# Kernel optimization log

Hardware: AMD Instinct MI355X
Metric: run time of the kernel (lower is better)

Reference implementation:

```python
import jax, jax.numpy as jnp
import numpy as np

N = 100000
E = 1600000
NIN = 128
NOUT = 128


def setup_inputs() -> dict:
    key = jax.random.key(0)
    k1, k2, k3, k4 = jax.random.split(key, 4)
    x = jax.random.normal(k1, (N, NIN), dtype=jnp.float32)
    edge_index = jax.random.randint(k2, (2, E), 0, N, dtype=jnp.int64)
    edge_attr = jnp.ones((E,), dtype=jnp.float32)  # unused by GCNConv
    # PyG Linear weight is [out, in]; glorot-ish init
    W = jax.random.normal(k3, (NOUT, NIN), dtype=jnp.float32) / np.sqrt(NIN)
    b = jnp.zeros((NOUT,), dtype=jnp.float32)
    return {"x": x, "edge_index": edge_index, "edge_attr": edge_attr, "W": W, "b": b}


def reference(x, edge_index, edge_attr, W, b):
    # PyG GCNConv: add self-loops, symmetric degree normalization,
    # linear transform, scatter-add aggregation at destination, + bias.
    n = x.shape[0]
    loops = jnp.arange(n, dtype=edge_index.dtype)
    src = jnp.concatenate([edge_index[0], loops])  # [E+N]
    dst = jnp.concatenate([edge_index[1], loops])  # [E+N]
    # degree over destination (col) including self-loops, edge weight = 1
    deg = jax.ops.segment_sum(jnp.ones_like(dst, dtype=x.dtype), dst, num_segments=n)
    dinv = jnp.where(deg > 0, jax.lax.rsqrt(deg), 0.0)
    norm = dinv[src] * dinv[dst]  # [E+N]
    h = x @ W.T  # [N, NOUT]
    msg = h[src] * norm[:, None]  # [E+N, NOUT]
    out = jax.ops.segment_sum(msg, dst, num_segments=n)  # [N, NOUT]
    return out + b
```

## Files before the change

### kernel.cpp

```cpp
#include <hip/hip_runtime.h>

#define TPB 256
#define NSCAT 256
#define BSH 5
#define BCAP 1024
#define MAXBUK 3200

typedef __attribute__((ext_vector_type(4))) float f32x4;
typedef __attribute__((ext_vector_type(8))) short short8;

__device__ __forceinline__ unsigned short f2bf(float f) {
    unsigned u = __float_as_uint(f);
    u = (u + 0x7fffu + ((u >> 16) & 1u)) >> 16;
    return (unsigned short)u;
}
__device__ __forceinline__ float bflo(unsigned u) { return __uint_as_float(u << 16); }
__device__ __forceinline__ float bfhi(unsigned u) { return __uint_as_float(u & 0xffff0000u); }


__global__ __launch_bounds__(256) void k_scatgemm(
    const int* __restrict__ src, const int* __restrict__ dst,
    int* __restrict__ bcur, unsigned* __restrict__ packed,
    const float* __restrict__ x, const float* __restrict__ W,
    unsigned short* __restrict__ g, int N, int E, int NBUK)
{
    __shared__ __align__(16) char smem[34816];
    const int t = threadIdx.x;

    if (blockIdx.x < NSCAT) {
        int* cnt = (int*)smem;
        int* cur = cnt + MAXBUK;
        for (int i = t; i < NBUK; i += 256) cnt[i] = 0;
        __syncthreads();
        const int chunk = (E + NSCAT - 1) / NSCAT;
        const int lo = blockIdx.x * chunk;
        const int hi = min(E, lo + chunk);
        for (int e = lo + t; e < hi; e += 256)
            atomicAdd(&cnt[dst[e] >> BSH], 1);
        __syncthreads();
        for (int i = t; i < NBUK; i += 256) {
            int c = cnt[i];
            cur[i] = i * BCAP + (c ? atomicAdd(&bcur[i], c) : 0);
        }
        __syncthreads();
        for (int e = lo + t; e < hi; e += 256) {
            int d = dst[e];
            int bkt = d >> BSH;
            int pos = atomicAdd(&cur[bkt], 1);
            if (pos < bkt * BCAP + BCAP)
                packed[pos] = ((unsigned)src[e] << 8) | (unsigned)(d & 31);
        }
    } else {
        typedef unsigned short wb_t[136];
        wb_t* wb = (wb_t*)smem;

        for (int ch = t; ch < 2048; ch += 256) {
            int nrow = ch >> 4, k8 = (ch & 15) << 3;
            const float* wp = W + nrow * 128 + k8;
            float4 w0 = *(const float4*)wp;
            float4 w1 = *(const float4*)(wp + 4);
            union { unsigned short u[8]; uint4 q; } pk;
            pk.u[0] = f2bf(w0.x); pk.u[1] = f2bf(w0.y); pk.u[2] = f2bf(w0.z); pk.u[3] = f2bf(w0.w);
            pk.u[4] = f2bf(w1.x); pk.u[5] = f2bf(w1.y); pk.u[6] = f2bf(w1.z); pk.u[7] = f2bf(w1.w);
            *(uint4*)&wb[nrow][k8] = pk.q;
        }
        __syncthreads();

        const int lane = t & 63;
        const int wid  = t >> 6;
        const int l15  = lane & 15;
        const int quad = lane >> 4;
        const int row  = (blockIdx.x - NSCAT) * 64 + wid * 16 + l15;
        const int rowc = (row < N) ? row : (N - 1);

        f32x4 acc[8];
        #pragma unroll
        for (int u = 0; u < 8; ++u) acc[u] = (f32x4){0.f, 0.f, 0.f, 0.f};

        #pragma unroll
        for (int ks = 0; ks < 4; ++ks) {
            const int kb = ks * 32 + quad * 8;
            float4 a0 = *(const float4*)(x + (long)rowc * 128 + kb);
            float4 a1 = *(const float4*)(x + (long)rowc * 128 + kb + 4);
            union { unsigned short u[8]; short8 v; } af;
            af.u[0] = f2bf(a0.x); af.u[1] = f2bf(a0.y); af.u[2] = f2bf(a0.z); af.u[3] = f2bf(a0.w);
            af.u[4] = f2bf(a1.x); af.u[5] = f2bf(a1.y); af.u[6] = f2bf(a1.z); af.u[7] = f2bf(a1.w);
            #pragma unroll
            for (int u = 0; u < 8; ++u) {
                short8 bf = *(const short8*)&wb[u * 16 + l15][kb];
                acc[u] = __builtin_amdgcn_mfma_f32_16x16x32_bf16(bf, af.v, acc[u], 0, 0, 0);
            }
        }

        if (row < N) {
            unsigned short* gp = g + (long)row * 128 + quad * 4;
            #pragma unroll
            for (int u = 0; u < 8; ++u) {
                unsigned short u0 = f2bf(acc[u][0]);
                unsigned short u1 = f2bf(acc[u][1]);
                unsigned short u2 = f2bf(acc[u][2]);
                unsigned short u3 = f2bf(acc[u][3]);
                uint2 pk;
                pk.x = (unsigned)u0 | ((unsigned)u1 << 16);
                pk.y = (unsigned)u2 | ((unsigned)u3 << 16);
                *(uint2*)(gp + u * 16) = pk;
            }
        }
    }
}


__global__ __launch_bounds__(256) void k_dinv(const unsigned* __restrict__ packed,
                                              const int* __restrict__ bcur,
                                              float* __restrict__ dinv, int N) {
    __shared__ int hist[32];
    const int b = blockIdx.x;
    const int t = threadIdx.x;
    if (t < 32) hist[t] = 0;
    __syncthreads();
    const int cnt = min(bcur[b], BCAP);
    const int base = b * BCAP;
    for (int e = t; e < cnt; e += 256)
        atomicAdd(&hist[packed[base + e] & 31u], 1);
    __syncthreads();
    if (t < 32) {
        int d = (b << BSH) + t;
        if (d < N) dinv[d] = rsqrtf((float)hist[t] + 1.0f);
    }
}


__global__ __launch_bounds__(256) void k_aggsort(const unsigned* __restrict__ packed,
                                                 const int* __restrict__ bcur,
                                                 const float* __restrict__ dinv,
                                                 const unsigned short* __restrict__ g,
                                                 const float* __restrict__ b_,
                                                 float* __restrict__ out, int N) {
    __shared__ int hist[32], lbase[32], scur[32];
    __shared__ unsigned stage[BCAP];
    const int b = blockIdx.x;
    const int t = threadIdx.x;
    if (t < 32) hist[t] = 0;
    __syncthreads();
    const int cnt = min(bcur[b], BCAP);
    const int base = b * BCAP;
    for (int e = t; e < cnt; e += 256)
        atomicAdd(&hist[packed[base + e] & 31u], 1);
    __syncthreads();
    if (t < 32) {
        int v = hist[t];
        int incl = v;
        #pragma unroll
        for (int d = 1; d < 32; d <<= 1) {
            int o = __shfl_up(incl, d);
            if (t >= d) incl += o;
        }
        lbase[t] = incl - v;
        scur[t]  = incl - v;
    }
    __syncthreads();
    for (int e = t; e < cnt; e += 256) {
        unsigned pk = packed[base + e];
        int pos = atomicAdd(&scur[pk & 31u], 1);
        stage[pos] = pk & 0xffffff00u;
    }
    __syncthreads();

    const int c = (t & 31) << 2;
    const char* gb = (const char*)g + (c << 1);
    #pragma unroll 1
    for (int round = 0; round < 4; ++round) {
        const int dl = round * 8 + (t >> 5);
        const int d  = (b << BSH) + dl;
        if (d >= N) continue;

        float4 acc = make_float4(0.f, 0.f, 0.f, 0.f);
        auto addrow = [&](unsigned off) {
            float dv = dinv[off >> 8];
            uint2 p = *(const uint2*)(gb + off);
            acc.x = fmaf(bflo(p.x), dv, acc.x);
            acc.y = fmaf(bfhi(p.x), dv, acc.y);
            acc.z = fmaf(bflo(p.y), dv, acc.z);
            acc.w = fmaf(bfhi(p.y), dv, acc.w);
        };

        addrow((unsigned)d << 8);
        int e  = lbase[dl];
        int s1 = e + hist[dl];
        for (; e + 8 <= s1; e += 8) {
            unsigned a[8];
            #pragma unroll
            for (int j = 0; j < 8; ++j) a[j] = stage[e + j];
            #pragma unroll
            for (int j = 0; j < 8; ++j) addrow(a[j]);
        }
        for (; e + 4 <= s1; e += 4) {
            unsigned a[4];
            #pragma unroll
            for (int j = 0; j < 4; ++j) a[j] = stage[e + j];
            #pragma unroll
            for (int j = 0; j < 4; ++j) addrow(a[j]);
        }
        for (; e < s1; ++e) addrow(stage[e]);

        float s = rsqrtf((float)hist[dl] + 1.0f);
        float4 bb = *(const float4*)(b_ + c);
        float4 r = make_float4(acc.x * s + bb.x, acc.y * s + bb.y,
                               acc.z * s + bb.z, acc.w * s + bb.w);
        *(float4*)(out + (long)d * 128 + c) = r;
    }
}


extern "C" void kernel_launch(void* const* d_in, const int* in_sizes, int n_in,
                              void* d_out, int out_size, void* d_ws, size_t ws_size,
                              hipStream_t stream) {
    const float* x  = (const float*)d_in[0];
    const int*   ei = (const int*)d_in[1];
    const float* W  = (const float*)d_in[3];
    const float* b  = (const float*)d_in[4];
    float* out = (float*)d_out;

    const int N = in_sizes[0] / 128;
    const int E = in_sizes[1] / 2;
    const int* src = ei;
    const int* dst = ei + E;
    const int NBUK = (N + 31) >> BSH;

    char* p = (char*)d_ws;
    auto carve = [&](size_t bytes) { char* q = p; p += (bytes + 255) & ~(size_t)255; return q; };
    int*            bcur   = (int*)           carve((size_t)MAXBUK * 4);
    float*          dinv   = (float*)         carve((size_t)N * 4);
    unsigned*       packed = (unsigned*)      carve((size_t)MAXBUK * BCAP * 4);
    unsigned short* g      = (unsigned short*)carve((size_t)N * 128 * 2);

    const int gemmBlocks = (N + 63) / 64;

    hipMemsetAsync(bcur, 0, (size_t)NBUK * 4, stream);

    k_scatgemm<<<NSCAT + gemmBlocks, TPB, 0, stream>>>(src, dst, bcur, packed,
                                                       x, W, g, N, E, NBUK);
    k_dinv    <<<NBUK, TPB, 0, stream>>>(packed, bcur, dinv, N);
    k_aggsort <<<NBUK, TPB, 0, stream>>>(packed, bcur, dinv, g, b, out, N);
}
```

Baseline: 230.5 us.

## Halve shared memory by staging W in two halves and reusing scatter buffer

Cuts the kernel's static shared memory in half. The scatter path now keeps bucket counts and cursors in a single array, and the GEMM path converts and stages W into LDS one 64-row half at a time, with an extra pair of barriers per half. The x row fragments are loaded and converted once up front and held in registers. The aim is higher occupancy (more resident blocks per CU); the cost is extra synchronisation and more live registers.

```diff
diff --git a/kernel.cpp b/kernel.cpp
--- a/kernel.cpp
+++ b/kernel.cpp
@@ -24,47 +24,34 @@
     const float* __restrict__ x, const float* __restrict__ W,
     unsigned short* __restrict__ g, int N, int E, int NBUK)
 {
-    __shared__ __align__(16) char smem[34816];
+    __shared__ __align__(16) char smem[17408];
     const int t = threadIdx.x;
 
     if (blockIdx.x < NSCAT) {
-        int* cnt = (int*)smem;
-        int* cur = cnt + MAXBUK;
-        for (int i = t; i < NBUK; i += 256) cnt[i] = 0;
+        int* a = (int*)smem;
+        for (int i = t; i < NBUK; i += 256) a[i] = 0;
         __syncthreads();
         const int chunk = (E + NSCAT - 1) / NSCAT;
         const int lo = blockIdx.x * chunk;
         const int hi = min(E, lo + chunk);
         for (int e = lo + t; e < hi; e += 256)
-            atomicAdd(&cnt[dst[e] >> BSH], 1);
+            atomicAdd(&a[dst[e] >> BSH], 1);
         __syncthreads();
         for (int i = t; i < NBUK; i += 256) {
-            int c = cnt[i];
-            cur[i] = i * BCAP + (c ? atomicAdd(&bcur[i], c) : 0);
+            int c = a[i];
+            a[i] = i * BCAP + (c ? atomicAdd(&bcur[i], c) : 0);
         }
         __syncthreads();
         for (int e = lo + t; e < hi; e += 256) {
             int d = dst[e];
             int bkt = d >> BSH;
-            int pos = atomicAdd(&cur[bkt], 1);
+            int pos = atomicAdd(&a[bkt], 1);
             if (pos < bkt * BCAP + BCAP)
                 packed[pos] = ((unsigned)src[e] << 8) | (unsigned)(d & 31);
         }
     } else {
         typedef unsigned short wb_t[136];
         wb_t* wb = (wb_t*)smem;
-
-        for (int ch = t; ch < 2048; ch += 256) {
-            int nrow = ch >> 4, k8 = (ch & 15) << 3;
-            const float* wp = W + nrow * 128 + k8;
-            float4 w0 = *(const float4*)wp;
-            float4 w1 = *(const float4*)(wp + 4);
-            union { unsigned short u[8]; uint4 q; } pk;
-            pk.u[0] = f2bf(w0.x); pk.u[1] = f2bf(w0.y); pk.u[2] = f2bf(w0.z); pk.u[3] = f2bf(w0.w);
-            pk.u[4] = f2bf(w1.x); pk.u[5] = f2bf(w1.y); pk.u[6] = f2bf(w1.z); pk.u[7] = f2bf(w1.w);
-            *(uint4*)&wb[nrow][k8] = pk.q;
-        }
-        __syncthreads();
 
         const int lane = t & 63;
         const int wid  = t >> 6;
@@ -73,23 +60,46 @@
         const int row  = (blockIdx.x - NSCAT) * 64 + wid * 16 + l15;
         const int rowc = (row < N) ? row : (N - 1);
 
-        f32x4 acc[8];
-        #pragma unroll
-        for (int u = 0; u < 8; ++u) acc[u] = (f32x4){0.f, 0.f, 0.f, 0.f};
-
+        short8 af[4];
         #pragma unroll
         for (int ks = 0; ks < 4; ++ks) {
             const int kb = ks * 32 + quad * 8;
             float4 a0 = *(const float4*)(x + (long)rowc * 128 + kb);
             float4 a1 = *(const float4*)(x + (long)rowc * 128 + kb + 4);
-            union { unsigned short u[8]; short8 v; } af;
-            af.u[0] = f2bf(a0.x); af.u[1] = f2bf(a0.y); af.u[2] = f2bf(a0.z); af.u[3] = f2bf(a0.w);
-            af.u[4] = f2bf(a1.x); af.u[5] = f2bf(a1.y); af.u[6] = f2bf(a1.z); af.u[7] = f2bf(a1.w);
-            #pragma unroll
-            for (int u = 0; u < 8; ++u) {
-                short8 bf = *(const short8*)&wb[u * 16 + l15][kb];
-                acc[u] = __builtin_amdgcn_mfma_f32_16x16x32_bf16(bf, af.v, acc[u], 0, 0, 0);
+            union { unsigned short u[8]; short8 v; } cf;
+            cf.u[0] = f2bf(a0.x); cf.u[1] = f2bf(a0.y); cf.u[2] = f2bf(a0.z); cf.u[3] = f2bf(a0.w);
+            cf.u[4] = f2bf(a1.x); cf.u[5] = f2bf(a1.y); cf.u[6] = f2bf(a1.z); cf.u[7] = f2bf(a1.w);
+            af[ks] = cf.v;
+        }
+
+        f32x4 acc[8];
+        #pragma unroll
+        for (int u = 0; u < 8; ++u) acc[u] = (f32x4){0.f, 0.f, 0.f, 0.f};
+
+        #pragma unroll
+        for (int half = 0; half < 2; ++half) {
+            for (int ch = t; ch < 1024; ch += 256) {
+                int nrow = ch >> 4, k8 = (ch & 15) << 3;
+                const float* wp = W + (half * 64 + nrow) * 128 + k8;
+                float4 w0 = *(const float4*)wp;
+                float4 w1 = *(const float4*)(wp + 4);
+                union { unsigned short u[8]; uint4 q; } pk;
+                pk.u[0] = f2bf(w0.x); pk.u[1] = f2bf(w0.y); pk.u[2] = f2bf(w0.z); pk.u[3] = f2bf(w0.w);
+                pk.u[4] = f2bf(w1.x); pk.u[5] = f2bf(w1.y); pk.u[6] = f2bf(w1.z); pk.u[7] = f2bf(w1.w);
+                *(uint4*)&wb[nrow][k8] = pk.q;
             }
+            __syncthreads();
+            #pragma unroll
+            for (int ks = 0; ks < 4; ++ks) {
+                const int kb = ks * 32 + quad * 8;
+                #pragma unroll
+                for (int u = 0; u < 4; ++u) {
+                    short8 bf = *(const short8*)&wb[u * 16 + l15][kb];
+                    acc[half * 4 + u] =
+                        __builtin_amdgcn_mfma_f32_16x16x32_bf16(bf, af[ks], acc[half * 4 + u], 0, 0, 0);
+                }
+            }
+            __syncthreads();
         }
 
         if (row < N) {
```

Result: no change. 233.7 us (+1.4%).
